# Optimization experiments

Hardware: AMD Instinct MI355X
Metric: run time of the kernel (lower is better)

The kernel has to match this reference:

```python
import jax, jax.numpy as jnp
import numpy as np

EPS = 1e-5

def layer_norm(x, g, b):
    mu = jnp.mean(x, axis=-1, keepdims=True)
    var = jnp.mean(jnp.square(x - mu), axis=-1, keepdims=True)
    return (x - mu) * jax.lax.rsqrt(var + EPS) * g + b

def gather_recent(seq_tokens, seq_mask, count):
    # vectorized right-aligned gather of last `count` valid tokens per row
    B, S, D = seq_tokens.shape
    csum = jnp.cumsum(seq_mask.astype(jnp.int32), axis=1)          # [B,S]
    total = csum[:, -1:]                                           # [B,1]
    rank = total - csum                                            # 0 = last valid (at valid positions)
    sel = seq_mask & (rank < count)
    dest = jnp.where(sel, count - 1 - rank, count)                 # dump invalid into slot `count`
    b_idx = jnp.arange(B)[:, None]
    buf = jnp.zeros((B, count + 1, D), seq_tokens.dtype)
    recent = buf.at[b_idx, dest].set(seq_tokens * sel[..., None].astype(seq_tokens.dtype))[:, :count]
    recent_mask = jnp.arange(count)[None, :] >= (count - total)    # [B,count]
    return recent, recent_mask

def setup_inputs() -> dict:
    key = jax.random.key(0)
    B, S, D, H, P = 16, 2048, 1024, 16, 8
    ks = jax.random.split(key, 8)
    hidden_states = jax.random.normal(ks[0], (B, S, D), jnp.float32)
    lengths = jax.random.randint(ks[1], (B,), 1, S + 1)
    valid_mask = jnp.arange(S)[None, :] < lengths[:, None]
    s = 0.02
    return {
        "hidden_states": hidden_states,
        "valid_mask": valid_mask,
        "queries": jax.random.normal(ks[2], (P, D), jnp.float32) * s,
        "in_proj_w": jax.random.normal(ks[3], (3 * D, D), jnp.float32) * s,
        "in_proj_b": jnp.zeros((3 * D,), jnp.float32),
        "out_w": jax.random.normal(ks[4], (D, D), jnp.float32) * s,
        "out_b": jnp.zeros((D,), jnp.float32),
        "ln_pma_g": jnp.ones((D,), jnp.float32),
        "ln_pma_b": jnp.zeros((D,), jnp.float32),
        "ln_v_g": jnp.ones((D,), jnp.float32),
        "ln_v_b": jnp.zeros((D,), jnp.float32),
        "W_v": jax.random.normal(ks[5], (D, D), jnp.float32) * s,
        "b_v": jnp.zeros((D,), jnp.float32),
        "ln_g_g": jnp.ones((D,), jnp.float32),
        "ln_g_b": jnp.zeros((D,), jnp.float32),
        "W_g": jax.random.normal(ks[6], (D, D), jnp.float32) * s,
        "b_g": jnp.zeros((D,), jnp.float32),
        "cls_count": 1, "pma_count": 8, "recent_count": 64, "num_heads": 16,
    }

def reference(hidden_states, valid_mask, queries, in_proj_w, in_proj_b, out_w, out_b,
              ln_pma_g, ln_pma_b, ln_v_g, ln_v_b, W_v, b_v, ln_g_g, ln_g_b, W_g, b_g,
              cls_count, pma_count, recent_count, num_heads):
    B, S, D = hidden_states.shape
    H = num_heads
    hd = D // H
    # ---- PMA (torch nn.MultiheadAttention, batch_first, eval/no-dropout) ----
    Wq, Wk, Wv_ = in_proj_w[:D], in_proj_w[D:2 * D], in_proj_w[2 * D:]
    bq, bk, bv_ = in_proj_b[:D], in_proj_b[D:2 * D], in_proj_b[2 * D:]
    q = (queries @ Wq.T + bq)                       # [P, D]
    k = hidden_states @ Wk.T + bk                   # [B, S, D]
    v = hidden_states @ Wv_.T + bv_                 # [B, S, D]
    qh = q.reshape(pma_count, H, hd)                # [P, H, hd]
    kh = k.reshape(B, S, H, hd)
    vh = v.reshape(B, S, H, hd)
    scores = jnp.einsum('phd,bshd->bhps', qh, kh) / jnp.sqrt(jnp.asarray(hd, hidden_states.dtype))
    scores = jnp.where(valid_mask[:, None, None, :], scores, jnp.asarray(-1e9, scores.dtype))
    attn = jax.nn.softmax(scores, axis=-1)          # [B, H, P, S]
    ctx = jnp.einsum('bhps,bshd->bphd', attn, vh).reshape(B, pma_count, D)
    pooled = ctx @ out_w.T + out_b
    pma_tokens = layer_norm(queries[None, :, :] + pooled, ln_pma_g, ln_pma_b)  # [B, P, D]
    pma_mask = jnp.ones((B, pma_count), bool)
    # ---- split cls / sequence, gather recent ----
    cls_tokens = hidden_states[:, :cls_count]
    cls_mask = valid_mask[:, :cls_count]
    recent_tokens, recent_mask = gather_recent(hidden_states[:, cls_count:],
                                               valid_mask[:, cls_count:], recent_count)
    summary = jnp.concatenate([cls_tokens, pma_tokens, recent_tokens], axis=1)
    summary_mask = jnp.concatenate([cls_mask, pma_mask, recent_mask], axis=1)
    # ---- SiLU self-gating ----
    val = jax.nn.silu(layer_norm(summary, ln_v_g, ln_v_b) @ W_v.T + b_v)
    gate = jax.nn.sigmoid(layer_norm(summary, ln_g_g, ln_g_b) @ W_g.T + b_g)
    gated = gate * val * summary_mask[..., None].astype(summary.dtype)
    return gated, summary_mask
```

## Files before the change

kernel.cpp:

```cpp
#include <hip/hip_runtime.h>
#include <hip/hip_bf16.h>
#include <math.h>


#define Bn 16
#define Sn 2048
#define Dn 1024
#define Hn 16
#define Pn 8
#define Tn 73
#define RECn 64

typedef __attribute__((ext_vector_type(8))) short short8;
typedef __attribute__((ext_vector_type(4))) float f32x4;

__device__ __forceinline__ short f2bf(float x) {
    union { __hip_bfloat16 h; short s; } u;
    u.h = __float2bfloat16(x);
    return u.s;
}

__global__ void detect_mask_kernel(const unsigned char* __restrict__ raw,
                                   int* __restrict__ flag) {
    __shared__ int any;
    if (threadIdx.x == 0) any = 0;
    __syncthreads();
    const uint4* r4 = (const uint4*)raw;
    int local = 0;
    for (int i = threadIdx.x; i < (Bn * Sn) / 16; i += blockDim.x) {
        uint4 w = r4[i];
        if ((w.x & 0xFFFFFF00u) | (w.y & 0xFFFFFF00u) |
            (w.z & 0xFFFFFF00u) | (w.w & 0xFFFFFF00u)) local = 1;
    }
    if (local) any = 1;
    __syncthreads();
    if (threadIdx.x == 0) *flag = any;
}

__global__ void canon_mask_kernel(const void* __restrict__ raw,
                                  const int* __restrict__ flag,
                                  unsigned char* __restrict__ canon) {
    int i = blockIdx.x * blockDim.x + threadIdx.x;
    if (i >= Bn * Sn) return;
    unsigned char v;
    if (*flag)
        v = ((const unsigned char*)raw)[i] ? 1 : 0;
    else
        v = ((const int*)raw)[i] ? 1 : 0;
    canon[i] = v;
}

__global__ void prep_kernel(const unsigned char* __restrict__ valid,
                            int* __restrict__ totals, int* __restrict__ rsrc,
                            float* __restrict__ maskf) {
    int b = blockIdx.x, t = threadIdx.x;
    const int SP = Sn - 1;
    __shared__ int lc[256];
    if (t < RECn) rsrc[b * RECn + t] = -1;

    int base = t * 8;
    unsigned char m[8];
    int cnt = 0;
#pragma unroll
    for (int i = 0; i < 8; i++) {
        int idx = base + i;
        m[i] = (idx < SP) ? valid[(size_t)b * Sn + 1 + idx] : (unsigned char)0;
        cnt += m[i] ? 1 : 0;
    }
    lc[t] = cnt;
    __syncthreads();
    for (int off = 1; off < 256; off <<= 1) {
        int add = (t >= off) ? lc[t - off] : 0;
        __syncthreads();
        lc[t] += add;
        __syncthreads();
    }
    int total = lc[255];
    int run = lc[t] - cnt;
#pragma unroll
    for (int i = 0; i < 8; i++) {
        if (m[i]) {
            run++;
            int rank = total - run;
            if (rank < RECn) rsrc[b * RECn + (RECn - 1 - rank)] = base + i + 1;
        }
    }
    if (t == 0) totals[b] = total;
    if (t < Tn) {
        float mv;
        if (t == 0) mv = valid[(size_t)b * Sn] ? 1.0f : 0.0f;
        else if (t < 1 + Pn) mv = 1.0f;
        else mv = ((t - 9) >= RECn - total) ? 1.0f : 0.0f;
        maskf[b * Tn + t] = mv;
    }
}

__global__ void q_kernel(const float* __restrict__ queries,
                         const float* __restrict__ in_w,
                         const float* __restrict__ in_b,
                         float* __restrict__ q) {
    int wid = (blockIdx.x * blockDim.x + threadIdx.x) >> 6;
    int lane = threadIdx.x & 63;
    if (wid >= Pn * Dn) return;
    int p = wid >> 10, j = wid & 1023;
    float acc = 0.0f;
    for (int c = lane; c < Dn; c += 64)
        acc += queries[p * Dn + c] * in_w[(size_t)j * Dn + c];
#pragma unroll
    for (int off = 32; off > 0; off >>= 1) acc += __shfl_down(acc, off);
    if (lane == 0) q[wid] = acc + in_b[j];
}

__global__ void A_kernel(const float* __restrict__ q,
                         const float* __restrict__ in_w,
                         const float* __restrict__ in_b,
                         short* __restrict__ Amat_bf, float* __restrict__ c0) {
    int h = blockIdx.x, cblk = blockIdx.y;
    int c = cblk * 256 + threadIdx.x;
    __shared__ float qs[8][64];
    for (int i = threadIdx.x; i < 512; i += 256) {
        int p = i >> 6, d = i & 63;
        qs[p][d] = q[p * Dn + h * 64 + d];
    }
    __syncthreads();
    float acc[8] = {};
#pragma unroll 8
    for (int d = 0; d < 64; d++) {
        float w = in_w[(size_t)(Dn + h * 64 + d) * Dn + c];
#pragma unroll
        for (int p = 0; p < 8; p++) acc[p] = fmaf(qs[p][d], w, acc[p]);
    }
#pragma unroll
    for (int p = 0; p < 8; p++)
        Amat_bf[(size_t)(h * 8 + p) * Dn + c] = f2bf(acc[p] * 0.125f);
    if (cblk == 0 && threadIdx.x < 8) {
        int p = threadIdx.x;
        float a = 0.0f;
        for (int d = 0; d < 64; d++) a += qs[p][d] * in_b[Dn + h * 64 + d];
        c0[h * 8 + p] = a * 0.125f;
    }
}

__global__ void wcvt_kernel(const float* __restrict__ w, short* __restrict__ wbf, int n) {
    int i = (blockIdx.x * blockDim.x + threadIdx.x) * 8;
    if (i >= n) return;
    f32x4 x0 = *(const f32x4*)(w + i);
    f32x4 x1 = *(const f32x4*)(w + i + 4);
    short8 o;
#pragma unroll
    for (int j = 0; j < 4; j++) { o[j] = f2bf(x0[j]); o[j + 4] = f2bf(x1[j]); }
    *(short8*)(wbf + i) = o;
}

__global__ __launch_bounds__(256) void scores_mfma(const float* __restrict__ hidden,
                                                   const short* __restrict__ Amat_bf,
                                                   const float* __restrict__ c0,
                                                   const unsigned char* __restrict__ valid,
                                                   float* __restrict__ scores) {
    int tid = threadIdx.x, wave = tid >> 6, lane = tid & 63;
    int l15 = lane & 15, koff = (lane >> 4) * 8;
    int mrow0 = blockIdx.x * 64 + wave * 16;
    int b = mrow0 >> 11, s_base = mrow0 & 2047;

    __shared__ short Ab[2][128][40];
    int shp = tid >> 1, skp = (tid & 1) * 16;
    const short* aglob = Amat_bf + (size_t)shp * Dn + skp;
    const float* hptr = hidden + (size_t)(mrow0 + l15) * Dn + koff;

    f32x4 acc[8] = {};
    {
        short8 s0 = *(const short8*)(aglob);
        short8 s1 = *(const short8*)(aglob + 8);
        *(short8*)(&Ab[0][shp][skp]) = s0;
        *(short8*)(&Ab[0][shp][skp + 8]) = s1;
    }
    f32x4 ha = *(const f32x4*)(hptr);
    f32x4 hb = *(const f32x4*)(hptr + 4);
    f32x4 ha1 = *(const f32x4*)(hptr + 32);
    f32x4 hb1 = *(const f32x4*)(hptr + 36);

    for (int ic = 0; ic < 32; ic++) {
        int cur = ic & 1;
        short8 nA0 = {}, nA1 = {};
        f32x4 nh0 = {}, nh1 = {};
        if (ic + 1 < 32) {
            nA0 = *(const short8*)(aglob + (ic + 1) * 32);
            nA1 = *(const short8*)(aglob + (ic + 1) * 32 + 8);
        }
        if (ic + 2 < 32) {
            nh0 = *(const f32x4*)(hptr + (ic + 2) * 32);
            nh1 = *(const f32x4*)(hptr + (ic + 2) * 32 + 4);
        }
        __syncthreads();
        short8 av;
#pragma unroll
        for (int i = 0; i < 4; i++) { av[i] = f2bf(ha[i]); av[i + 4] = f2bf(hb[i]); }
#pragma unroll
        for (int nt = 0; nt < 8; nt++) {
            short8 bv = *(const short8*)(&Ab[cur][nt * 16 + l15][koff]);
            acc[nt] = __builtin_amdgcn_mfma_f32_16x16x32_bf16(av, bv, acc[nt], 0, 0, 0);
        }
        if (ic + 1 < 32) {
            *(short8*)(&Ab[cur ^ 1][shp][skp]) = nA0;
            *(short8*)(&Ab[cur ^ 1][shp][skp + 8]) = nA1;
        }
        ha = ha1; hb = hb1; ha1 = nh0; hb1 = nh1;
    }
    int srow = s_base + (lane >> 4) * 4;
    const unsigned char* vptr = valid + (size_t)b * Sn + srow;
    bool ok0 = vptr[0] != 0, ok1 = vptr[1] != 0, ok2 = vptr[2] != 0, ok3 = vptr[3] != 0;
#pragma unroll
    for (int nt = 0; nt < 8; nt++) {
        int hp = nt * 16 + l15;
        float cc = c0[hp];
        f32x4 st;
        st[0] = ok0 ? acc[nt][0] + cc : -1.0e9f;
        st[1] = ok1 ? acc[nt][1] + cc : -1.0e9f;
        st[2] = ok2 ? acc[nt][2] + cc : -1.0e9f;
        st[3] = ok3 ? acc[nt][3] + cc : -1.0e9f;
        *(f32x4*)(scores + (size_t)(b * 128 + hp) * Sn + srow) = st;
    }
}

__global__ __launch_bounds__(256) void softmax_kernel(const float* __restrict__ scores,
                                                      short* __restrict__ attn_bf) {
    const float* row = scores + (size_t)blockIdx.x * Sn;
    short* orow = attn_bf + (size_t)blockIdx.x * Sn;
    int t = threadIdx.x;
    __shared__ float red[256];
    f32x4 v0 = *(const f32x4*)(row + t * 8);
    f32x4 v1 = *(const f32x4*)(row + t * 8 + 4);
    float mx = -1.0e30f;
#pragma unroll
    for (int i = 0; i < 4; i++) { mx = fmaxf(mx, v0[i]); mx = fmaxf(mx, v1[i]); }
    red[t] = mx;
    __syncthreads();
    for (int off = 128; off > 0; off >>= 1) {
        if (t < off) red[t] = fmaxf(red[t], red[t + off]);
        __syncthreads();
    }
    mx = red[0];
    __syncthreads();
    float e[8];
    float sum = 0.0f;
#pragma unroll
    for (int i = 0; i < 4; i++) {
        e[i] = expf(v0[i] - mx); sum += e[i];
        e[i + 4] = expf(v1[i] - mx); sum += e[i + 4];
    }
    red[t] = sum;
    __syncthreads();
    for (int off = 128; off > 0; off >>= 1) {
        if (t < off) red[t] += red[t + off];
        __syncthreads();
    }
    float inv = 1.0f / red[0];
    short8 o;
#pragma unroll
    for (int i = 0; i < 8; i++) o[i] = f2bf(e[i] * inv);
    *(short8*)(orow + t * 8) = o;
}

__global__ __launch_bounds__(512) void U_mfma(const short* __restrict__ attn_bf,
                                              const float* __restrict__ hidden,
                                              float* __restrict__ Up0,
                                              float* __restrict__ Up1,
                                              float* __restrict__ Up2) {
    int b = blockIdx.y, n0 = blockIdx.x * 64, z = blockIdx.z;
    int zbase = z * 704;
    int zlen = (z == 2) ? 640 : 704;
    float* Up = (z == 0) ? Up0 : (z == 1) ? Up1 : Up2;

    int tid = threadIdx.x, wave = tid >> 6, lane = tid & 63;
    int l15 = lane & 15;
    __shared__ short ldsB[2][64][40];
    int kr = tid & 31, nc = ((tid >> 5) & 15) * 4;
    int koff = (lane >> 4) * 8;
    f32x4 acc[4] = {};
    const short* aBase = attn_bf + ((size_t)b * 128 + wave * 16 + l15) * Sn + zbase + koff;
    const float* hBase = hidden + ((size_t)b * Sn + zbase + kr) * Dn + n0 + nc;

    int nk = zlen >> 5;
    f32x4 h = *(const f32x4*)(hBase);
#pragma unroll
    for (int i = 0; i < 4; i++) ldsB[0][nc + i][kr] = f2bf(h[i]);
    short8 av = *(const short8*)(aBase);

    for (int ic = 0; ic < nk; ic++) {
        int cur = ic & 1;
        bool more = (ic + 1 < nk);
        f32x4 hn;
        short8 avn;
        if (more) {
            hn = *(const f32x4*)(hBase + (size_t)(ic + 1) * 32 * Dn);
            avn = *(const short8*)(aBase + (ic + 1) * 32);
        }
        __syncthreads();
#pragma unroll
        for (int nf = 0; nf < 4; nf++) {
            short8 bv = *(const short8*)(&ldsB[cur][nf * 16 + l15][koff]);
            acc[nf] = __builtin_amdgcn_mfma_f32_16x16x32_bf16(av, bv, acc[nf], 0, 0, 0);
        }
        if (more) {
#pragma unroll
            for (int i = 0; i < 4; i++) ldsB[cur ^ 1][nc + i][kr] = f2bf(hn[i]);
            av = avn;
        }
    }
    int hp = wave * 16 + (lane >> 4) * 4;
#pragma unroll
    for (int nf = 0; nf < 4; nf++) {
        int c = n0 + nf * 16 + l15;
        float* up = Up + (size_t)(b * 128 + hp) * Dn + c;
#pragma unroll
        for (int r = 0; r < 4; r++) up[(size_t)r * Dn] = acc[nf][r];
    }
}

__global__ __launch_bounds__(64) void ctx_mfma(const float* __restrict__ Up0,
                                               const float* __restrict__ Up1,
                                               const float* __restrict__ Up2,
                                               const float* __restrict__ in_w,
                                               const float* __restrict__ in_b,
                                               float* __restrict__ ctx) {
    int bh = blockIdx.x, b = bh >> 4, h = bh & 15;
    int lane = threadIdx.x & 63, l15 = lane & 15, koff = (lane >> 4) * 8;
    int p = l15 & 7;
    size_t uoff = ((size_t)b * 128 + h * 8 + p) * Dn + koff;
    const float* wv = in_w + (size_t)(2 * Dn + h * 64 + l15) * Dn + koff;
    f32x4 acc[4] = {};
    for (int k0 = 0; k0 < Dn; k0 += 32) {
        f32x4 a0 = *(const f32x4*)(Up0 + uoff + k0);
        f32x4 a1 = *(const f32x4*)(Up0 + uoff + k0 + 4);
        f32x4 b0 = *(const f32x4*)(Up1 + uoff + k0);
        f32x4 b1 = *(const f32x4*)(Up1 + uoff + k0 + 4);
        f32x4 d0 = *(const f32x4*)(Up2 + uoff + k0);
        f32x4 d1 = *(const f32x4*)(Up2 + uoff + k0 + 4);
        short8 av;
#pragma unroll
        for (int i = 0; i < 4; i++) {
            av[i] = f2bf(a0[i] + b0[i] + d0[i]);
            av[i + 4] = f2bf(a1[i] + b1[i] + d1[i]);
        }
#pragma unroll
        for (int nt = 0; nt < 4; nt++) {
            f32x4 w0 = *(const f32x4*)(wv + (size_t)nt * 16 * Dn + k0);
            f32x4 w1 = *(const f32x4*)(wv + (size_t)nt * 16 * Dn + k0 + 4);
            short8 bv;
#pragma unroll
            for (int i = 0; i < 4; i++) { bv[i] = f2bf(w0[i]); bv[i + 4] = f2bf(w1[i]); }
            acc[nt] = __builtin_amdgcn_mfma_f32_16x16x32_bf16(av, bv, acc[nt], 0, 0, 0);
        }
    }
    if (lane < 32) {
        int prow = (lane >> 4) * 4;
#pragma unroll
        for (int nt = 0; nt < 4; nt++) {
            int d = h * 64 + nt * 16 + l15;
            float bias = in_b[2 * Dn + d];
#pragma unroll
            for (int r = 0; r < 4; r++)
                ctx[(size_t)(b * 8 + prow + r) * Dn + d] = acc[nt][r] + bias;
        }
    }
}

__global__ __launch_bounds__(256) void pooled_mfma(const float* __restrict__ A,
                                                   const float* __restrict__ B,
                                                   const float* __restrict__ bias,
                                                   float* __restrict__ C, int M) {
    int wave = threadIdx.x >> 6, lane = threadIdx.x & 63;
    int l15 = lane & 15, koff = (lane >> 4) * 8;
    int m0 = blockIdx.x * 64 + (wave >> 1) * 32;
    int n0 = blockIdx.y * 64 + (wave & 1) * 32;
    f32x4 acc[2][2] = {};
    int ra0 = min(m0 + l15, M - 1);
    int ra1 = min(m0 + 16 + l15, M - 1);
    const float* a0p = A + (size_t)ra0 * Dn + koff;
    const float* a1p = A + (size_t)ra1 * Dn + koff;
    const float* b0p = B + (size_t)(n0 + l15) * Dn + koff;
    const float* b1p = B + (size_t)(n0 + 16 + l15) * Dn + koff;
    for (int k0 = 0; k0 < Dn; k0 += 32) {
        short8 av0, av1, bv0, bv1;
        f32x4 x, y;
        x = *(const f32x4*)(a0p + k0); y = *(const f32x4*)(a0p + k0 + 4);
#pragma unroll
        for (int i = 0; i < 4; i++) { av0[i] = f2bf(x[i]); av0[i + 4] = f2bf(y[i]); }
        x = *(const f32x4*)(a1p + k0); y = *(const f32x4*)(a1p + k0 + 4);
#pragma unroll
        for (int i = 0; i < 4; i++) { av1[i] = f2bf(x[i]); av1[i + 4] = f2bf(y[i]); }
        x = *(const f32x4*)(b0p + k0); y = *(const f32x4*)(b0p + k0 + 4);
#pragma unroll
        for (int i = 0; i < 4; i++) { bv0[i] = f2bf(x[i]); bv0[i + 4] = f2bf(y[i]); }
        x = *(const f32x4*)(b1p + k0); y = *(const f32x4*)(b1p + k0 + 4);
#pragma unroll
        for (int i = 0; i < 4; i++) { bv1[i] = f2bf(x[i]); bv1[i + 4] = f2bf(y[i]); }
        acc[0][0] = __builtin_amdgcn_mfma_f32_16x16x32_bf16(av0, bv0, acc[0][0], 0, 0, 0);
        acc[0][1] = __builtin_amdgcn_mfma_f32_16x16x32_bf16(av0, bv1, acc[0][1], 0, 0, 0);
        acc[1][0] = __builtin_amdgcn_mfma_f32_16x16x32_bf16(av1, bv0, acc[1][0], 0, 0, 0);
        acc[1][1] = __builtin_amdgcn_mfma_f32_16x16x32_bf16(av1, bv1, acc[1][1], 0, 0, 0);
    }
#pragma unroll
    for (int mf = 0; mf < 2; mf++) {
        int row0 = m0 + mf * 16 + (lane >> 4) * 4;
#pragma unroll
        for (int nf = 0; nf < 2; nf++) {
            int col = n0 + nf * 16 + l15;
            float bval = bias[col];
#pragma unroll
            for (int r = 0; r < 4; r++) {
                int row = row0 + r;
                if (row < M) C[(size_t)row * Dn + col] = acc[mf][nf][r] + bval;
            }
        }
    }
}

__global__ __launch_bounds__(256) void wgemm_mfma(const short* __restrict__ Abf,
                                                  const short* __restrict__ Bbf,
                                                  const float* __restrict__ bias,
                                                  float* __restrict__ C, int M) {
    int wave = threadIdx.x >> 6, lane = threadIdx.x & 63;
    int m0 = blockIdx.x * 64 + (wave >> 1) * 32;
    int n0 = blockIdx.y * 64 + (wave & 1) * 32;
    int koff = (lane >> 4) * 8;
    f32x4 acc[2][2] = {};
    int ra0 = min(m0 + (lane & 15), M - 1);
    int ra1 = min(m0 + 16 + (lane & 15), M - 1);
    const short* a0p = Abf + (size_t)ra0 * Dn + koff;
    const short* a1p = Abf + (size_t)ra1 * Dn + koff;
    const short* b0p = Bbf + (size_t)(n0 + (lane & 15)) * Dn + koff;
    const short* b1p = Bbf + (size_t)(n0 + 16 + (lane & 15)) * Dn + koff;
    for (int k0 = 0; k0 < Dn; k0 += 32) {
        short8 av0 = *(const short8*)(a0p + k0);
        short8 av1 = *(const short8*)(a1p + k0);
        short8 bv0 = *(const short8*)(b0p + k0);
        short8 bv1 = *(const short8*)(b1p + k0);
        acc[0][0] = __builtin_amdgcn_mfma_f32_16x16x32_bf16(av0, bv0, acc[0][0], 0, 0, 0);
        acc[0][1] = __builtin_amdgcn_mfma_f32_16x16x32_bf16(av0, bv1, acc[0][1], 0, 0, 0);
        acc[1][0] = __builtin_amdgcn_mfma_f32_16x16x32_bf16(av1, bv0, acc[1][0], 0, 0, 0);
        acc[1][1] = __builtin_amdgcn_mfma_f32_16x16x32_bf16(av1, bv1, acc[1][1], 0, 0, 0);
    }
#pragma unroll
    for (int mf = 0; mf < 2; mf++) {
        int row0 = m0 + mf * 16 + (lane >> 4) * 4;
#pragma unroll
        for (int nf = 0; nf < 2; nf++) {
            int col = n0 + nf * 16 + (lane & 15);
            float bval = bias[col];
#pragma unroll
            for (int r = 0; r < 4; r++) {
                int row = row0 + r;
                if (row < M) C[(size_t)row * Dn + col] = acc[mf][nf][r] + bval;
            }
        }
    }
}

__device__ __forceinline__ float block_sum(float v, float* red) {
    int tid = threadIdx.x;
    red[tid] = v;
    __syncthreads();
    for (int off = 128; off > 0; off >>= 1) {
        if (tid < off) red[tid] += red[tid + off];
        __syncthreads();
    }
    float r = red[0];
    __syncthreads();
    return r;
}

__global__ void summary_ln_kernel(const float* __restrict__ hidden,
                                  const float* __restrict__ queries,
                                  const float* __restrict__ pooled,
                                  const int* __restrict__ rsrc,
                                  const float* __restrict__ gpma, const float* __restrict__ bpma,
                                  const float* __restrict__ gv, const float* __restrict__ bv,
                                  const float* __restrict__ gg, const float* __restrict__ bg,
                                  short* __restrict__ lnv, short* __restrict__ lng) {
    __shared__ float red[256];
    int b = blockIdx.x, t = blockIdx.y, tid = threadIdx.x;
    float x[4];
    if (t == 0) {
#pragma unroll
        for (int i = 0; i < 4; i++)
            x[i] = hidden[(size_t)b * Sn * Dn + tid + i * 256];
    } else if (t < 1 + Pn) {
        int p = t - 1;
#pragma unroll
        for (int i = 0; i < 4; i++) {
            int c = tid + i * 256;
            x[i] = queries[p * Dn + c] + pooled[((size_t)b * Pn + p) * Dn + c];
        }
    } else {
        int src = rsrc[b * RECn + (t - 9)];
        if (src >= 0) {
#pragma unroll
            for (int i = 0; i < 4; i++)
                x[i] = hidden[((size_t)b * Sn + src) * Dn + tid + i * 256];
        } else {
#pragma unroll
            for (int i = 0; i < 4; i++) x[i] = 0.0f;
        }
    }
    if (t >= 1 && t < 1 + Pn) {
        float mu = block_sum(x[0] + x[1] + x[2] + x[3], red) * (1.0f / Dn);
        float d2 = 0.0f;
#pragma unroll
        for (int i = 0; i < 4; i++) { float d = x[i] - mu; d2 += d * d; }
        float inv = rsqrtf(block_sum(d2, red) * (1.0f / Dn) + 1e-5f);
#pragma unroll
        for (int i = 0; i < 4; i++) {
            int c = tid + i * 256;
            x[i] = (x[i] - mu) * inv * gpma[c] + bpma[c];
        }
    }
    float mu = block_sum(x[0] + x[1] + x[2] + x[3], red) * (1.0f / Dn);
    float d2 = 0.0f;
#pragma unroll
    for (int i = 0; i < 4; i++) { float d = x[i] - mu; d2 += d * d; }
    float inv = rsqrtf(block_sum(d2, red) * (1.0f / Dn) + 1e-5f);
    size_t row = (size_t)(b * Tn + t) * Dn;
#pragma unroll
    for (int i = 0; i < 4; i++) {
        int c = tid + i * 256;
        float xh = (x[i] - mu) * inv;
        lnv[row + c] = f2bf(xh * gv[c] + bv[c]);
        lng[row + c] = f2bf(xh * gg[c] + bg[c]);
    }
}

__global__ void gated_kernel(const float* __restrict__ c1, const float* __restrict__ c2,
                             const float* __restrict__ maskf, float* __restrict__ out) {
    int gi = blockIdx.x * blockDim.x + threadIdx.x;
    int row = gi >> 10;
    float m = maskf[row];
    float a = c1[gi], g = c2[gi];
    float sv = a / (1.0f + expf(-a));
    float sg = 1.0f / (1.0f + expf(-g));
    out[gi] = sg * sv * m;
}

extern "C" void kernel_launch(void* const* d_in, const int* in_sizes, int n_in,
                              void* d_out, int out_size, void* d_ws, size_t ws_size,
                              hipStream_t stream) {
    const float* hidden = (const float*)d_in[0];
    const void* valid_raw = d_in[1];
    const float* queries = (const float*)d_in[2];
    const float* in_w = (const float*)d_in[3];
    const float* in_b = (const float*)d_in[4];
    const float* out_w = (const float*)d_in[5];
    const float* out_b = (const float*)d_in[6];
    const float* ln_pma_g = (const float*)d_in[7];
    const float* ln_pma_b = (const float*)d_in[8];
    const float* ln_v_g = (const float*)d_in[9];
    const float* ln_v_b = (const float*)d_in[10];
    const float* W_v = (const float*)d_in[11];
    const float* b_v = (const float*)d_in[12];
    const float* ln_g_g = (const float*)d_in[13];
    const float* ln_g_b = (const float*)d_in[14];
    const float* W_g = (const float*)d_in[15];
    const float* b_g = (const float*)d_in[16];

    float* ws = (float*)d_ws;
    float* out = (float*)d_out;

    float* SC      = ws;
    short* attn_bf = (short*)(ws + 4194304);
    float* Up0     = ws + 6291456;
    float* Up1     = ws;
    float* Up2     = ws + 2097152;
    float* qbuf    = ws + 8388608;
    short* Amat_bf = (short*)(ws + 8396800);
    float* c0      = ws + 8462336;
    float* ctx     = ws + 8462592;
    float* pooled  = ws + 8593664;
    short* Wv_bf   = (short*)(ws + 8724736);
    short* Wg_bf   = (short*)(ws + 9249024);
    int*   ivals   = (int*)(ws + 9773312);
    int* totals = ivals;
    int* rsrc = ivals + 16;
    int* flag = ivals + 16 + 1024;
    unsigned char* canon = (unsigned char*)(ivals + 16 + 1024 + 16);
    short* lnv_bf = (short*)ws;
    short* lng_bf = (short*)(ws + 622592);
    float* c1 = ws + 1245184;
    float* c2 = ws + 2441216;
    float* maskf = out + (size_t)Bn * Tn * Dn;

    const int M2 = Bn * Tn;

    detect_mask_kernel<<<1, 256, 0, stream>>>((const unsigned char*)valid_raw, flag);
    canon_mask_kernel<<<(Bn * Sn) / 256, 256, 0, stream>>>(valid_raw, flag, canon);
    prep_kernel<<<Bn, 256, 0, stream>>>(canon, totals, rsrc, maskf);
    q_kernel<<<(Pn * Dn) / 4, 256, 0, stream>>>(queries, in_w, in_b, qbuf);
    A_kernel<<<dim3(Hn, 4), 256, 0, stream>>>(qbuf, in_w, in_b, Amat_bf, c0);
    wcvt_kernel<<<512, 256, 0, stream>>>(W_v, Wv_bf, Dn * Dn);
    wcvt_kernel<<<512, 256, 0, stream>>>(W_g, Wg_bf, Dn * Dn);
    scores_mfma<<<(Bn * Sn) / 64, 256, 0, stream>>>(hidden, Amat_bf, c0, canon, SC);
    softmax_kernel<<<Bn * 128, 256, 0, stream>>>(SC, attn_bf);
    U_mfma<<<dim3(16, Bn, 3), 512, 0, stream>>>(attn_bf, hidden, Up0, Up1, Up2);
    ctx_mfma<<<Bn * Hn, 64, 0, stream>>>(Up0, Up1, Up2, in_w, in_b, ctx);
    pooled_mfma<<<dim3(2, 16), 256, 0, stream>>>(ctx, out_w, out_b, pooled, Bn * Pn);
    summary_ln_kernel<<<dim3(Bn, Tn), 256, 0, stream>>>(hidden, queries, pooled, rsrc,
                                                        ln_pma_g, ln_pma_b, ln_v_g, ln_v_b,
                                                        ln_g_g, ln_g_b, lnv_bf, lng_bf);
    wgemm_mfma<<<dim3((M2 + 63) / 64, 16), 256, 0, stream>>>(lnv_bf, Wv_bf, b_v, c1, M2);
    wgemm_mfma<<<dim3((M2 + 63) / 64, 16), 256, 0, stream>>>(lng_bf, Wg_bf, b_g, c2, M2);
    gated_kernel<<<(Bn * Tn * Dn) / 256, 256, 0, stream>>>(c1, c2, maskf, out);
}
```

Before: 239.3 us.

## Retile scores and U GEMMs: split heads across waves, widen U tiles, 4-way K split

The scores kernel now gives each block 32 rows instead of 64. Pairs of waves share one row tile and each covers half of the 128 head-query columns, which doubles the grid and halves the accumulators per wave. The U kernel widens the N tile to 128 columns, so each hidden tile converted to bf16 feeds twice as many outputs. It also splits the sequence into four 512-long chunks with a fourth partial buffer, which ctx_mfma sums. The aim is more parallelism in scores and fewer redundant hidden reads and conversions in U. The cost is extra workspace, one more partial buffer to reduce, and hidden rows being reloaded by both waves of a pair in scores.

```diff
diff --git a/kernel.cpp b/kernel.cpp
--- a/kernel.cpp
+++ b/kernel.cpp
@@ -159,7 +159,8 @@
                                                    float* __restrict__ scores) {
     int tid = threadIdx.x, wave = tid >> 6, lane = tid & 63;
     int l15 = lane & 15, koff = (lane >> 4) * 8;
-    int mrow0 = blockIdx.x * 64 + wave * 16;
+    int mrow0 = blockIdx.x * 32 + (wave >> 1) * 16;
+    int hpbase = (wave & 1) * 64;
     int b = mrow0 >> 11, s_base = mrow0 & 2047;
 
     __shared__ short Ab[2][128][40];
@@ -167,7 +168,7 @@
     const short* aglob = Amat_bf + (size_t)shp * Dn + skp;
     const float* hptr = hidden + (size_t)(mrow0 + l15) * Dn + koff;
 
-    f32x4 acc[8] = {};
+    f32x4 acc[4] = {};
     {
         short8 s0 = *(const short8*)(aglob);
         short8 s1 = *(const short8*)(aglob + 8);
@@ -196,8 +197,8 @@
 #pragma unroll
         for (int i = 0; i < 4; i++) { av[i] = f2bf(ha[i]); av[i + 4] = f2bf(hb[i]); }
 #pragma unroll
-        for (int nt = 0; nt < 8; nt++) {
-            short8 bv = *(const short8*)(&Ab[cur][nt * 16 + l15][koff]);
+        for (int nt = 0; nt < 4; nt++) {
+            short8 bv = *(const short8*)(&Ab[cur][hpbase + nt * 16 + l15][koff]);
             acc[nt] = __builtin_amdgcn_mfma_f32_16x16x32_bf16(av, bv, acc[nt], 0, 0, 0);
         }
         if (ic + 1 < 32) {
@@ -210,8 +211,8 @@
     const unsigned char* vptr = valid + (size_t)b * Sn + srow;
     bool ok0 = vptr[0] != 0, ok1 = vptr[1] != 0, ok2 = vptr[2] != 0, ok3 = vptr[3] != 0;
 #pragma unroll
-    for (int nt = 0; nt < 8; nt++) {
-        int hp = nt * 16 + l15;
+    for (int nt = 0; nt < 4; nt++) {
+        int hp = hpbase + nt * 16 + l15;
         float cc = c0[hp];
         f32x4 st;
         st[0] = ok0 ? acc[nt][0] + cc : -1.0e9f;
@@ -265,51 +266,59 @@
                                               const float* __restrict__ hidden,
                                               float* __restrict__ Up0,
                                               float* __restrict__ Up1,
-                                              float* __restrict__ Up2) {
-    int b = blockIdx.y, n0 = blockIdx.x * 64, z = blockIdx.z;
-    int zbase = z * 704;
-    int zlen = (z == 2) ? 640 : 704;
-    float* Up = (z == 0) ? Up0 : (z == 1) ? Up1 : Up2;
+                                              float* __restrict__ Up2,
+                                              float* __restrict__ Up3) {
+    int b = blockIdx.y, n0 = blockIdx.x * 128, z = blockIdx.z;
+    int zbase = z * 512;
+    float* Up = (z == 0) ? Up0 : (z == 1) ? Up1 : (z == 2) ? Up2 : Up3;
 
     int tid = threadIdx.x, wave = tid >> 6, lane = tid & 63;
     int l15 = lane & 15;
-    __shared__ short ldsB[2][64][40];
-    int kr = tid & 31, nc = ((tid >> 5) & 15) * 4;
+    __shared__ short ldsB[2][128][40];
+    int kr = tid & 31, nc = (tid >> 5) * 8;
     int koff = (lane >> 4) * 8;
-    f32x4 acc[4] = {};
+    f32x4 acc[8] = {};
     const short* aBase = attn_bf + ((size_t)b * 128 + wave * 16 + l15) * Sn + zbase + koff;
     const float* hBase = hidden + ((size_t)b * Sn + zbase + kr) * Dn + n0 + nc;
 
-    int nk = zlen >> 5;
-    f32x4 h = *(const f32x4*)(hBase);
-#pragma unroll
-    for (int i = 0; i < 4; i++) ldsB[0][nc + i][kr] = f2bf(h[i]);
+    const int nk = 16;
+    f32x4 h0 = *(const f32x4*)(hBase);
+    f32x4 h1 = *(const f32x4*)(hBase + 4);
+#pragma unroll
+    for (int i = 0; i < 4; i++) {
+        ldsB[0][nc + i][kr] = f2bf(h0[i]);
+        ldsB[0][nc + 4 + i][kr] = f2bf(h1[i]);
+    }
     short8 av = *(const short8*)(aBase);
 
     for (int ic = 0; ic < nk; ic++) {
         int cur = ic & 1;
         bool more = (ic + 1 < nk);
-        f32x4 hn;
+        f32x4 hn0, hn1;
         short8 avn;
         if (more) {
-            hn = *(const f32x4*)(hBase + (size_t)(ic + 1) * 32 * Dn);
+            hn0 = *(const f32x4*)(hBase + (size_t)(ic + 1) * 32 * Dn);
+            hn1 = *(const f32x4*)(hBase + (size_t)(ic + 1) * 32 * Dn + 4);
             avn = *(const short8*)(aBase + (ic + 1) * 32);
         }
         __syncthreads();
 #pragma unroll
-        for (int nf = 0; nf < 4; nf++) {
+        for (int nf = 0; nf < 8; nf++) {
             short8 bv = *(const short8*)(&ldsB[cur][nf * 16 + l15][koff]);
             acc[nf] = __builtin_amdgcn_mfma_f32_16x16x32_bf16(av, bv, acc[nf], 0, 0, 0);
         }
         if (more) {
 #pragma unroll
-            for (int i = 0; i < 4; i++) ldsB[cur ^ 1][nc + i][kr] = f2bf(hn[i]);
+            for (int i = 0; i < 4; i++) {
+                ldsB[cur ^ 1][nc + i][kr] = f2bf(hn0[i]);
+                ldsB[cur ^ 1][nc + 4 + i][kr] = f2bf(hn1[i]);
+            }
             av = avn;
         }
     }
     int hp = wave * 16 + (lane >> 4) * 4;
 #pragma unroll
-    for (int nf = 0; nf < 4; nf++) {
+    for (int nf = 0; nf < 8; nf++) {
         int c = n0 + nf * 16 + l15;
         float* up = Up + (size_t)(b * 128 + hp) * Dn + c;
 #pragma unroll
@@ -320,6 +329,7 @@
 __global__ __launch_bounds__(64) void ctx_mfma(const float* __restrict__ Up0,
                                                const float* __restrict__ Up1,
                                                const float* __restrict__ Up2,
+                                               const float* __restrict__ Up3,
                                                const float* __restrict__ in_w,
                                                const float* __restrict__ in_b,
                                                float* __restrict__ ctx) {
@@ -336,11 +346,13 @@
         f32x4 b1 = *(const f32x4*)(Up1 + uoff + k0 + 4);
         f32x4 d0 = *(const f32x4*)(Up2 + uoff + k0);
         f32x4 d1 = *(const f32x4*)(Up2 + uoff + k0 + 4);
+        f32x4 e0 = *(const f32x4*)(Up3 + uoff + k0);
+        f32x4 e1 = *(const f32x4*)(Up3 + uoff + k0 + 4);
         short8 av;
 #pragma unroll
         for (int i = 0; i < 4; i++) {
-            av[i] = f2bf(a0[i] + b0[i] + d0[i]);
-            av[i + 4] = f2bf(a1[i] + b1[i] + d1[i]);
+            av[i] = f2bf((a0[i] + b0[i]) + (d0[i] + e0[i]));
+            av[i + 4] = f2bf((a1[i] + b1[i]) + (d1[i] + e1[i]));
         }
 #pragma unroll
         for (int nt = 0; nt < 4; nt++) {
@@ -570,14 +582,15 @@
     float* Up0     = ws + 6291456;
     float* Up1     = ws;
     float* Up2     = ws + 2097152;
-    float* qbuf    = ws + 8388608;
-    short* Amat_bf = (short*)(ws + 8396800);
-    float* c0      = ws + 8462336;
-    float* ctx     = ws + 8462592;
-    float* pooled  = ws + 8593664;
-    short* Wv_bf   = (short*)(ws + 8724736);
-    short* Wg_bf   = (short*)(ws + 9249024);
-    int*   ivals   = (int*)(ws + 9773312);
+    float* Up3     = ws + 8388608;
+    float* qbuf    = ws + 10485760;
+    short* Amat_bf = (short*)(ws + 10493952);
+    float* c0      = ws + 10559488;
+    float* ctx     = ws + 10559744;
+    float* pooled  = ws + 10690816;
+    short* Wv_bf   = (short*)(ws + 10821888);
+    short* Wg_bf   = (short*)(ws + 11346176);
+    int*   ivals   = (int*)(ws + 11870464);
     int* totals = ivals;
     int* rsrc = ivals + 16;
     int* flag = ivals + 16 + 1024;
@@ -597,10 +610,10 @@
     A_kernel<<<dim3(Hn, 4), 256, 0, stream>>>(qbuf, in_w, in_b, Amat_bf, c0);
     wcvt_kernel<<<512, 256, 0, stream>>>(W_v, Wv_bf, Dn * Dn);
     wcvt_kernel<<<512, 256, 0, stream>>>(W_g, Wg_bf, Dn * Dn);
-    scores_mfma<<<(Bn * Sn) / 64, 256, 0, stream>>>(hidden, Amat_bf, c0, canon, SC);
+    scores_mfma<<<(Bn * Sn) / 32, 256, 0, stream>>>(hidden, Amat_bf, c0, canon, SC);
     softmax_kernel<<<Bn * 128, 256, 0, stream>>>(SC, attn_bf);
-    U_mfma<<<dim3(16, Bn, 3), 512, 0, stream>>>(attn_bf, hidden, Up0, Up1, Up2);
-    ctx_mfma<<<Bn * Hn, 64, 0, stream>>>(Up0, Up1, Up2, in_w, in_b, ctx);
+    U_mfma<<<dim3(8, Bn, 4), 512, 0, stream>>>(attn_bf, hidden, Up0, Up1, Up2, Up3);
+    ctx_mfma<<<Bn * Hn, 64, 0, stream>>>(Up0, Up1, Up2, Up3, in_w, in_b, ctx);
     pooled_mfma<<<dim3(2, 16), 256, 0, stream>>>(ctx, out_w, out_b, pooled, Bn * Pn);
     summary_ln_kernel<<<dim3(Bn, Tn), 256, 0, stream>>>(hidden, queries, pooled, rsrc,
                                                         ln_pma_g, ln_pma_b, ln_v_g, ln_v_b,
```

Result: slower. 260.2 us (+8.7%).
